# Performance work log

Hardware: AMD Instinct MI355X
Metric: run time of the kernel (lower is better)

The kernel has to match this reference:

```python
import jax, jax.numpy as jnp
import numpy as np

B, S, D = 4, 1024, 2048
NH, HD = 16, 128  # nhead, head_dim
SCALE = HD ** -0.5


def setup_inputs() -> dict:
    key = jax.random.key(0)
    ks = jax.random.split(key, 7)
    query = jax.random.normal(ks[0], (B, S, D), dtype=jnp.float32)
    key_t = jax.random.normal(ks[1], (B, S, D), dtype=jnp.float32)
    value = jax.random.normal(ks[2], (B, S, D), dtype=jnp.float32)
    # qkv_proj: Linear(D, 3D) with bias; out_proj: Linear(D, D) with bias
    Wqkv = jax.random.normal(ks[3], (3 * D, D), dtype=jnp.float32) * (D ** -0.5)
    bqkv = jnp.zeros((3 * D,), dtype=jnp.float32)
    Wout = jax.random.normal(ks[4], (D, D), dtype=jnp.float32) * (D ** -0.5)
    bout = jnp.zeros((D,), dtype=jnp.float32)
    return {"query": query, "key": key_t, "value": value,
            "Wqkv": Wqkv, "bqkv": bqkv, "Wout": Wout, "bout": bout}


def reference(query, key, value, Wqkv, bqkv, Wout, bout):
    # NOTE: module ignores `key`/`value` args; qkv comes from query alone.
    b, s, d = query.shape
    qkv = query @ Wqkv.T + bqkv                       # (B,S,3D)
    q, k, v = jnp.split(qkv, 3, axis=-1)
    q = q.reshape(b, s, NH, HD).transpose(0, 2, 1, 3) * SCALE  # (B,H,S,hd)
    k = k.reshape(b, s, NH, HD).transpose(0, 2, 1, 3)          # (B,H,S,hd)
    # faithful replication of the module's odd v permutation:
    v = v.reshape(b, s, HD, NH).transpose(0, 2, 1, 3)          # (B,hd,S,H)
    v = v.reshape(b, s, NH * HD).reshape(b, s, NH, HD).transpose(0, 2, 1, 3)  # (B,H,S,hd)
    scores = jnp.einsum('bhqd,bhkd->bhqk', q, k)               # (B,H,S,S)
    causal = jnp.triu(jnp.ones((s, s), dtype=bool), k=1)
    scores = jnp.where(causal, -jnp.inf, scores)
    attn = jax.nn.softmax(scores.astype(jnp.float32), axis=-1).astype(query.dtype)
    out = jnp.einsum('bhqk,bhkd->bhqd', attn, v)               # (B,H,S,hd)
    out = out.transpose(0, 2, 1, 3).reshape(b, s, d)
    return out @ Wout.T + bout
```

## Files before the change

### kernel.cpp

```cpp
#include <hip/hip_runtime.h>
#include <hip/hip_bf16.h>
#include <stdint.h>

typedef __bf16 bf16x8 __attribute__((ext_vector_type(8)));
typedef float  floatx4 __attribute__((ext_vector_type(4)));

#define NEG_BIG (-1e30f)

#define GLD16(g, l) __builtin_amdgcn_global_load_lds(                         \
    (__attribute__((address_space(1))) void*)(g),                             \
    (__attribute__((address_space(3))) void*)(l), 16, 0, 0)

__device__ __forceinline__ void cvt16(const float* __restrict__ s,
                                      __hip_bfloat16* __restrict__ d) {
    float4 f[4];
#pragma unroll
    for (int i = 0; i < 4; i++) f[i] = ((const float4*)s)[i];
    union { __hip_bfloat16 h[16]; uint4 u[2]; } o;
#pragma unroll
    for (int i = 0; i < 4; i++) {
        o.h[4 * i + 0] = __float2bfloat16(f[i].x);
        o.h[4 * i + 1] = __float2bfloat16(f[i].y);
        o.h[4 * i + 2] = __float2bfloat16(f[i].z);
        o.h[4 * i + 3] = __float2bfloat16(f[i].w);
    }
    ((uint4*)d)[0] = o.u[0];
    ((uint4*)d)[1] = o.u[1];
}

__global__ __launch_bounds__(256)
void cvt3_f32_bf16(const float* __restrict__ a, size_t na8,
                   const float* __restrict__ b, size_t nb8,
                   const float* __restrict__ c, size_t nc8,
                   __hip_bfloat16* __restrict__ da,
                   __hip_bfloat16* __restrict__ db,
                   __hip_bfloat16* __restrict__ dc)
{
    const size_t total  = na8 + nb8 + nc8;
    const size_t stride = (size_t)gridDim.x * blockDim.x;
    for (size_t idx = (size_t)blockIdx.x * blockDim.x + threadIdx.x;
         idx < total; idx += stride) {
        const float* s; __hip_bfloat16* d; size_t o;
        if (idx < na8)            { s = a; d = da; o = idx; }
        else if (idx < na8 + nb8) { s = b; d = db; o = idx - na8; }
        else                      { s = c; d = dc; o = idx - na8 - nb8; }
        const float4 f0 = ((const float4*)s)[o * 2 + 0];
        const float4 f1 = ((const float4*)s)[o * 2 + 1];
        union { __hip_bfloat16 h[8]; uint4 u; } z;
        z.h[0] = __float2bfloat16(f0.x); z.h[1] = __float2bfloat16(f0.y);
        z.h[2] = __float2bfloat16(f0.z); z.h[3] = __float2bfloat16(f0.w);
        z.h[4] = __float2bfloat16(f1.x); z.h[5] = __float2bfloat16(f1.y);
        z.h[6] = __float2bfloat16(f1.z); z.h[7] = __float2bfloat16(f1.w);
        ((uint4*)d)[o] = z.u;
    }
}

__global__ __launch_bounds__(256, 2)
void gemm2b_nt_bias(const __hip_bfloat16* __restrict__ A,
                    const __hip_bfloat16* __restrict__ B,
                    const float* __restrict__ bias,
                    __hip_bfloat16* __restrict__ C,
                    int M, int N, int K, int lda, int ldb)
{
    __shared__ __align__(16) __hip_bfloat16 Asm[2][128 * 64];
    __shared__ __align__(16) __hip_bfloat16 Bsm[2][192 * 64];

    const int flat = blockIdx.x;
    const int c    = flat & 7;
    const int i_   = flat >> 3;
    const int by = (c & 1) * 16 + (i_ & 15);
    const int bx = (c >> 1) * 8 + (i_ >> 4);
    const int m0 = by * 128, n0 = bx * 192;

    const int t    = threadIdx.x;
    const int wave = t >> 6, lane = t & 63;
    const int quad = lane >> 4, l16 = lane & 15;
    const int wr   = wave >> 1, wc = wave & 1;
    const int NT   = K >> 6;

    const int l8 = lane >> 3;
    const int g_ = (lane & 7) ^ l8;
    auto stageA = [&](int tk, int j, int buf) {
        GLD16(A + (size_t)(m0 + j * 32 + wave * 8 + l8) * lda + tk * 64 + g_ * 8,
              &Asm[buf][0] + (j * 32 + wave * 8) * 64);
    };
    auto stageB = [&](int tk, int j, int buf) {
        GLD16(B + (size_t)(n0 + j * 32 + wave * 8 + l8) * ldb + tk * 64 + g_ * 8,
              &Bsm[buf][0] + (j * 32 + wave * 8) * 64);
    };

    const int g0 = (quad ^ (l16 & 7)) << 3;

    floatx4 acc[4][6];
    const floatx4 zero = {0.f, 0.f, 0.f, 0.f};
#pragma unroll
    for (int mi = 0; mi < 4; mi++)
#pragma unroll
        for (int ni = 0; ni < 6; ni++) acc[mi][ni] = zero;

#pragma unroll
    for (int j = 0; j < 4; j++) stageA(0, j, 0);
#pragma unroll
    for (int j = 0; j < 6; j++) stageB(0, j, 0);
    if (NT > 1) {
        stageA(1, 0, 1); stageA(1, 2, 1);
        stageB(1, 0, 1); stageB(1, 1, 1); stageB(1, 2, 1);
        asm volatile("s_waitcnt vmcnt(5)" ::: "memory");
    } else {
        asm volatile("s_waitcnt vmcnt(0)" ::: "memory");
    }
    __syncthreads();

    int cb = 0;
    for (int tk = 0; tk < NT; ++tk, cb ^= 1) {
        const __hip_bfloat16* Ab = &Asm[cb][0];
        const __hip_bfloat16* Bb = &Bsm[cb][0];
        const int nb = cb ^ 1;

        bf16x8 af[2][2], bfr[6][2];
#pragma unroll
        for (int i = 0; i < 2; i++)
#pragma unroll
            for (int ks = 0; ks < 2; ks++)
                af[i][ks] = *(const bf16x8*)(
                    Ab + (wr * 64 + i * 16 + l16) * 64 + (g0 ^ (ks ? 32 : 0)));
#pragma unroll
        for (int ni = 0; ni < 6; ni++)
#pragma unroll
            for (int ks = 0; ks < 2; ks++)
                bfr[ni][ks] = *(const bf16x8*)(
                    Bb + (wc * 96 + ni * 16 + l16) * 64 + (g0 ^ (ks ? 32 : 0)));
        if (tk + 1 < NT) {
            stageA(tk + 1, 1, nb); stageA(tk + 1, 3, nb);
            stageB(tk + 1, 3, nb); stageB(tk + 1, 4, nb); stageB(tk + 1, 5, nb);
        }
        __builtin_amdgcn_s_barrier();
        asm volatile("s_waitcnt lgkmcnt(0)" ::: "memory");
        __builtin_amdgcn_s_setprio(1);
#pragma unroll
        for (int ks = 0; ks < 2; ks++)
#pragma unroll
            for (int i = 0; i < 2; i++)
#pragma unroll
                for (int ni = 0; ni < 6; ni++)
                    acc[i][ni] = __builtin_amdgcn_mfma_f32_16x16x32_bf16(
                        af[i][ks], bfr[ni][ks], acc[i][ni], 0, 0, 0);
        __builtin_amdgcn_s_setprio(0);
        __builtin_amdgcn_s_barrier();

#pragma unroll
        for (int i = 0; i < 2; i++)
#pragma unroll
            for (int ks = 0; ks < 2; ks++)
                af[i][ks] = *(const bf16x8*)(
                    Ab + (wr * 64 + (2 + i) * 16 + l16) * 64 + (g0 ^ (ks ? 32 : 0)));
        if (tk + 2 < NT) {
            stageA(tk + 2, 0, cb); stageA(tk + 2, 2, cb);
            stageB(tk + 2, 0, cb); stageB(tk + 2, 1, cb); stageB(tk + 2, 2, cb);
        }
        __builtin_amdgcn_s_barrier();
        asm volatile("s_waitcnt lgkmcnt(0)" ::: "memory");
        __builtin_amdgcn_s_setprio(1);
#pragma unroll
        for (int ks = 0; ks < 2; ks++)
#pragma unroll
            for (int i = 0; i < 2; i++)
#pragma unroll
                for (int ni = 0; ni < 6; ni++)
                    acc[2 + i][ni] = __builtin_amdgcn_mfma_f32_16x16x32_bf16(
                        af[i][ks], bfr[ni][ks], acc[2 + i][ni], 0, 0, 0);
        __builtin_amdgcn_s_setprio(0);
        if (tk + 2 < NT)
            asm volatile("s_waitcnt vmcnt(5)" ::: "memory");
        else if (tk + 1 < NT)
            asm volatile("s_waitcnt vmcnt(0)" ::: "memory");
        __builtin_amdgcn_s_barrier();
    }

#pragma unroll
    for (int mi = 0; mi < 4; mi++) {
        const int row = m0 + wr * 64 + mi * 16 + quad * 4;
#pragma unroll
        for (int ni = 0; ni < 6; ni++) {
            const int col = n0 + wc * 96 + ni * 16 + l16;
            const float bv = bias[col];
#pragma unroll
            for (int r = 0; r < 4; r++)
                C[(size_t)(row + r) * N + col] =
                    __float2bfloat16(acc[mi][ni][r] + bv);
        }
    }
}

__global__ __launch_bounds__(256, 2)
void gemm2b128_nt_bias(const __hip_bfloat16* __restrict__ A,
                       const __hip_bfloat16* __restrict__ B,
                       const float* __restrict__ bias,
                       float* __restrict__ C,
                       int M, int N, int K, int lda, int ldb)
{
    __shared__ __align__(16) __hip_bfloat16 Asm[2][128 * 64];
    __shared__ __align__(16) __hip_bfloat16 Bsm[2][128 * 64];

    const int flat = blockIdx.x;
    const int c    = flat & 7;
    const int i_   = flat >> 3;
    const int by = (c & 3) * 8 + (i_ & 7);
    const int bx = (c >> 2) * 8 + (i_ >> 3);
    const int m0 = by * 128, n0 = bx * 128;

    const int t    = threadIdx.x;
    const int wave = t >> 6, lane = t & 63;
    const int quad = lane >> 4, l16 = lane & 15;
    const int wr   = wave >> 1, wc = wave & 1;
    const int NT   = K >> 6;

    const int l8 = lane >> 3;
    const int g_ = (lane & 7) ^ l8;
    auto stageA = [&](int tk, int j, int buf) {
        GLD16(A + (size_t)(m0 + j * 32 + wave * 8 + l8) * lda + tk * 64 + g_ * 8,
              &Asm[buf][0] + (j * 32 + wave * 8) * 64);
    };
    auto stageB = [&](int tk, int j, int buf) {
        GLD16(B + (size_t)(n0 + j * 32 + wave * 8 + l8) * ldb + tk * 64 + g_ * 8,
              &Bsm[buf][0] + (j * 32 + wave * 8) * 64);
    };

    const int g0 = (quad ^ (l16 & 7)) << 3;

    floatx4 acc[4][4];
    const floatx4 zero = {0.f, 0.f, 0.f, 0.f};
#pragma unroll
    for (int mi = 0; mi < 4; mi++)
#pragma unroll
        for (int ni = 0; ni < 4; ni++) acc[mi][ni] = zero;

#pragma unroll
    for (int j = 0; j < 4; j++) stageA(0, j, 0);
#pragma unroll
    for (int j = 0; j < 4; j++) stageB(0, j, 0);
    if (NT > 1) {
        stageA(1, 0, 1); stageA(1, 2, 1); stageB(1, 0, 1); stageB(1, 1, 1);
        asm volatile("s_waitcnt vmcnt(4)" ::: "memory");
    } else {
        asm volatile("s_waitcnt vmcnt(0)" ::: "memory");
    }
    __syncthreads();

    int cb = 0;
    for (int tk = 0; tk < NT; ++tk, cb ^= 1) {
        const __hip_bfloat16* Ab = &Asm[cb][0];
        const __hip_bfloat16* Bb = &Bsm[cb][0];
        const int nb = cb ^ 1;

        bf16x8 af[2][2], bfr[4][2];
#pragma unroll
        for (int i = 0; i < 2; i++)
#pragma unroll
            for (int ks = 0; ks < 2; ks++)
                af[i][ks] = *(const bf16x8*)(
                    Ab + (wr * 64 + i * 16 + l16) * 64 + (g0 ^ (ks ? 32 : 0)));
#pragma unroll
        for (int ni = 0; ni < 4; ni++)
#pragma unroll
            for (int ks = 0; ks < 2; ks++)
                bfr[ni][ks] = *(const bf16x8*)(
                    Bb + (wc * 64 + ni * 16 + l16) * 64 + (g0 ^ (ks ? 32 : 0)));
        if (tk + 1 < NT) {
            stageA(tk + 1, 1, nb); stageA(tk + 1, 3, nb);
            stageB(tk + 1, 2, nb); stageB(tk + 1, 3, nb);
        }
        __builtin_amdgcn_s_barrier();
        asm volatile("s_waitcnt lgkmcnt(0)" ::: "memory");
        __builtin_amdgcn_s_setprio(1);
#pragma unroll
        for (int ks = 0; ks < 2; ks++)
#pragma unroll
            for (int i = 0; i < 2; i++)
#pragma unroll
                for (int ni = 0; ni < 4; ni++)
                    acc[i][ni] = __builtin_amdgcn_mfma_f32_16x16x32_bf16(
                        af[i][ks], bfr[ni][ks], acc[i][ni], 0, 0, 0);
        __builtin_amdgcn_s_setprio(0);
        __builtin_amdgcn_s_barrier();

#pragma unroll
        for (int i = 0; i < 2; i++)
#pragma unroll
            for (int ks = 0; ks < 2; ks++)
                af[i][ks] = *(const bf16x8*)(
                    Ab + (wr * 64 + (2 + i) * 16 + l16) * 64 + (g0 ^ (ks ? 32 : 0)));
        if (tk + 2 < NT) {
            stageA(tk + 2, 0, cb); stageA(tk + 2, 2, cb);
            stageB(tk + 2, 0, cb); stageB(tk + 2, 1, cb);
        }
        __builtin_amdgcn_s_barrier();
        asm volatile("s_waitcnt lgkmcnt(0)" ::: "memory");
        __builtin_amdgcn_s_setprio(1);
#pragma unroll
        for (int ks = 0; ks < 2; ks++)
#pragma unroll
            for (int i = 0; i < 2; i++)
#pragma unroll
                for (int ni = 0; ni < 4; ni++)
                    acc[2 + i][ni] = __builtin_amdgcn_mfma_f32_16x16x32_bf16(
                        af[i][ks], bfr[ni][ks], acc[2 + i][ni], 0, 0, 0);
        __builtin_amdgcn_s_setprio(0);
        if (tk + 2 < NT)
            asm volatile("s_waitcnt vmcnt(4)" ::: "memory");
        else if (tk + 1 < NT)
            asm volatile("s_waitcnt vmcnt(0)" ::: "memory");
        __builtin_amdgcn_s_barrier();
    }

#pragma unroll
    for (int mi = 0; mi < 4; mi++) {
        const int row = m0 + wr * 64 + mi * 16 + quad * 4;
#pragma unroll
        for (int ni = 0; ni < 4; ni++) {
            const int col = n0 + wc * 64 + ni * 16 + l16;
            const float bv = bias[col];
#pragma unroll
            for (int r = 0; r < 4; r++)
                C[(size_t)(row + r) * N + col] = acc[mi][ni][r] + bv;
        }
    }
}

template <bool A_F32, bool B_F32, bool OUT_F32>
__global__ __launch_bounds__(256, 2)
void gemm_nt_bias(const void* __restrict__ Av, const void* __restrict__ Bv,
                  const float* __restrict__ bias, void* __restrict__ Cv,
                  int M, int N, int K, int lda, int ldb)
{
    __shared__ __align__(16) __hip_bfloat16 Asm[128 * 32];
    __shared__ __align__(16) __hip_bfloat16 Bsm[128 * 32];
    const int m0   = blockIdx.y * 128;
    const int n0   = blockIdx.x * 128;
    const int t    = threadIdx.x;
    const int wave = t >> 6, lane = t & 63;
    const int quad = lane >> 4, l16 = lane & 15;
    const int wr   = wave >> 1, wc = wave & 1;

    floatx4 zero = {0.f, 0.f, 0.f, 0.f};
    floatx4 acc[4][4];
    for (int i = 0; i < 4; i++)
        for (int j = 0; j < 4; j++) acc[i][j] = zero;

    for (int k0 = 0; k0 < K; k0 += 32) {
        if (A_F32) {
            const float* A = (const float*)Av;
            const int row = t >> 1, half = t & 1;
            cvt16(A + (size_t)(m0 + row) * lda + k0 + half * 16,
                  Asm + row * 32 + half * 16);
        } else {
            const __hip_bfloat16* A = (const __hip_bfloat16*)Av;
            for (int j = 0; j < 2; ++j) {
                const int chunk = (wave * 2 + j) * 64 + lane;
                const int row   = chunk >> 2;
                const int kc    = chunk & 3;
                GLD16(A + (size_t)(m0 + row) * lda + k0 + kc * 8,
                      Asm + (wave * 2 + j) * 512);
            }
        }
        if (B_F32) {
            const float* B = (const float*)Bv;
            const int row = t >> 1, half = t & 1;
            cvt16(B + (size_t)(n0 + row) * ldb + k0 + half * 16,
                  Bsm + row * 32 + half * 16);
        } else {
            const __hip_bfloat16* B = (const __hip_bfloat16*)Bv;
            for (int j = 0; j < 2; ++j) {
                const int chunk = (wave * 2 + j) * 64 + lane;
                const int row   = chunk >> 2;
                const int kc    = chunk & 3;
                GLD16(B + (size_t)(n0 + row) * ldb + k0 + kc * 8,
                      Bsm + (wave * 2 + j) * 512);
            }
        }
        __syncthreads();

        bf16x8 af[4], bf[4];
        for (int i = 0; i < 4; i++) {
            af[i] = *(const bf16x8*)(Asm + (wr * 64 + i * 16 + l16) * 32 + quad * 8);
            bf[i] = *(const bf16x8*)(Bsm + (wc * 64 + i * 16 + l16) * 32 + quad * 8);
        }
        for (int mi = 0; mi < 4; mi++)
            for (int ni = 0; ni < 4; ni++)
                acc[mi][ni] = __builtin_amdgcn_mfma_f32_16x16x32_bf16(
                    af[mi], bf[ni], acc[mi][ni], 0, 0, 0);
        __syncthreads();
    }

    for (int mi = 0; mi < 4; mi++) {
        const int row = m0 + wr * 64 + mi * 16 + quad * 4;
        for (int ni = 0; ni < 4; ni++) {
            const int col = n0 + wc * 64 + ni * 16 + l16;
            const float bv = bias[col];
            for (int r = 0; r < 4; r++) {
                const float v = acc[mi][ni][r] + bv;
                if (OUT_F32)
                    ((float*)Cv)[(size_t)(row + r) * N + col] = v;
                else
                    ((__hip_bfloat16*)Cv)[(size_t)(row + r) * N + col] =
                        __float2bfloat16(v);
            }
        }
    }
}

__global__ __launch_bounds__(256)
void permute_v(const __hip_bfloat16* __restrict__ QKV,
               __hip_bfloat16* __restrict__ Vpt)
{
    __shared__ __align__(16) __hip_bfloat16 S[64 * 64];
    const int blk = blockIdx.x;
    const int sb = blk & 31, h = (blk >> 5) & 15, b = blk >> 9;
    const int t = threadIdx.x;

    for (int j = 0; j < 2; j++) {
        const int chunk = j * 256 + t;
        const int lrow  = chunk >> 3;
        const int lcol  = (chunk & 7) * 8;
        const int r8 = lrow >> 3, jj = lrow & 7;
        const int srow = r8 * 128 + h * 8 + jj;
        const int scol = sb * 64 + lcol;
        *(uint4*)(S + chunk * 8) =
            *(const uint4*)(QKV + ((size_t)(b * 1024) + srow) * 6144 + 4096 + scol);
    }
    __syncthreads();

    const size_t obase = (((size_t)(b * 16 + h)) * 32 + sb) * 4096;
    for (int i = 0; i < 16; i++) {
        const int lin = t + 256 * i;
        const int hd = lin >> 5, ss = lin & 31;
        Vpt[obase + lin] =
            S[((ss & 7) * 8 + (hd >> 4)) * 64 + (ss >> 3) * 16 + (hd & 15)];
    }
}

__global__ __launch_bounds__(256, 2)
void flash_attn(const __hip_bfloat16* __restrict__ QKV,
                const __hip_bfloat16* __restrict__ Vpt,
                __hip_bfloat16* __restrict__ O)
{
    __shared__ __align__(16) __hip_bfloat16 Kt[2][64 * 128];
    __shared__ __align__(16) __hip_bfloat16 Vt[2][2 * 128 * 32];
    __shared__ __align__(16) __hip_bfloat16 Pl[64 * 64];

    const int bid  = blockIdx.x;
    const int pair = bid >> 6;
    const int g    = bid & 63;
    const int b    = g >> 4, h = g & 15;
    const int t    = threadIdx.x;
    const int wave = t >> 6, lane = t & 63;
    const int quad = lane >> 4, l16 = lane & 15;
    const float scale = 0.08838834764831845f;

    const int    rowb  = b * 1024;
    const size_t vbase = (((size_t)(b * 16 + h)) * 32) * 4096;
    const floatx4 zero = {0.f, 0.f, 0.f, 0.f};

    auto stageK = [&](int tk, int bufi) {
        const int kv0 = tk * 64;
        __hip_bfloat16* dst = &Kt[bufi][0];
#pragma unroll
        for (int j = 0; j < 4; j++) {
            const int c0 = (wave * 4 + j) * 64 + lane;
            const int r  = c0 >> 4;
            const int gg = (c0 & 15) ^ (r & 7);
            GLD16(QKV + ((size_t)(rowb + kv0 + r)) * 6144 + 2048 + h * 128 + gg * 8,
                  dst + (wave * 4 + j) * 512);
        }
    };
    auto stageV = [&](int tk, int bufi) {
        const __hip_bfloat16* src = Vpt + vbase + (size_t)(tk * 2) * 4096;
        __hip_bfloat16* dst = &Vt[bufi][0];
#pragma unroll
        for (int j = 0; j < 4; j++) {
            const int c0   = (wave * 4 + j) * 64 + lane;
            const int half = c0 >> 9, w = c0 & 511;
            const int r    = w >> 2;
            const int gg   = (w & 3) ^ (r & 3);
            GLD16(src + half * 4096 + r * 32 + gg * 8,
                  dst + (wave * 4 + j) * 512);
        }
    };

    for (int ph = 0; ph < 2; ++ph) {
        const int qb = ph ? (15 - pair) * 64 : pair * 64;
        const int nt = ph ? 16 - pair       : pair + 1;

        bf16x8 qf[4];
        {
            const size_t rb = ((size_t)(rowb + qb + wave * 16 + l16)) * 6144 + h * 128;
#pragma unroll
            for (int kc = 0; kc < 4; kc++)
                qf[kc] = *(const bf16x8*)(QKV + rb + kc * 32 + quad * 8);
        }

        float m_i[4], l_i[4];
        floatx4 oacc[8];
#pragma unroll
        for (int r = 0; r < 4; r++) { m_i[r] = NEG_BIG; l_i[r] = 0.f; }
#pragma unroll
        for (int ni = 0; ni < 8; ni++) oacc[ni] = zero;

        stageK(0, 0); stageV(0, 0);

        for (int tk = 0; tk < nt; ++tk) {
            const int cur = tk & 1;
            if (tk + 1 < nt) {
                stageK(tk + 1, cur ^ 1); stageV(tk + 1, cur ^ 1);
                asm volatile("s_waitcnt vmcnt(8)" ::: "memory");
            } else {
                asm volatile("s_waitcnt vmcnt(0)" ::: "memory");
            }
            __builtin_amdgcn_s_barrier();
            asm volatile("" ::: "memory");

            const __hip_bfloat16* Kb = &Kt[cur][0];
            const __hip_bfloat16* Vb = &Vt[cur][0];
            const int kv0 = tk * 64;

            floatx4 sc[4];
#pragma unroll
            for (int cbk = 0; cbk < 4; cbk++) {
                floatx4 s = zero;
                const int r  = cbk * 16 + l16;
                const int sw = r & 7;
#pragma unroll
                for (int kc = 0; kc < 4; kc++) {
                    bf16x8 kf = *(const bf16x8*)(
                        Kb + r * 128 + (((kc * 4 + quad) ^ sw) << 3));
                    s = __builtin_amdgcn_mfma_f32_16x16x32_bf16(qf[kc], kf, s, 0, 0, 0);
                }
                sc[cbk] = s;
            }

            const int qrow = qb + wave * 16 + quad * 4;
            if (tk == nt - 1) {
#pragma unroll
                for (int rr = 0; rr < 4; rr++)
#pragma unroll
                    for (int cbk = 0; cbk < 4; cbk++) {
                        const int col = kv0 + cbk * 16 + l16;
                        const float v = sc[cbk][rr] * scale;
                        sc[cbk][rr] = (col > qrow + rr) ? NEG_BIG : v;
                    }
            } else {
#pragma unroll
                for (int rr = 0; rr < 4; rr++)
#pragma unroll
                    for (int cbk = 0; cbk < 4; cbk++) sc[cbk][rr] *= scale;
            }
            float mx[4];
#pragma unroll
            for (int rr = 0; rr < 4; rr++)
                mx[rr] = fmaxf(fmaxf(sc[0][rr], sc[1][rr]),
                               fmaxf(sc[2][rr], sc[3][rr]));
#pragma unroll
            for (int off = 1; off < 16; off <<= 1)
#pragma unroll
                for (int rr = 0; rr < 4; rr++)
                    mx[rr] = fmaxf(mx[rr], __shfl_xor(mx[rr], off));

            bool grow = false;
#pragma unroll
            for (int rr = 0; rr < 4; rr++)
                grow = grow || (mx[rr] > m_i[rr] + 8.0f);
            if (__any((int)grow)) {
#pragma unroll
                for (int rr = 0; rr < 4; rr++) {
                    const float mnew  = fmaxf(m_i[rr], mx[rr]);
                    const float alpha = __expf(m_i[rr] - mnew);
                    m_i[rr] = mnew;
                    float lsum = 0.f;
#pragma unroll
                    for (int cbk = 0; cbk < 4; cbk++) {
                        const float pv = __expf(sc[cbk][rr] - mnew);
                        sc[cbk][rr] = pv;
                        lsum += pv;
                    }
                    l_i[rr] = l_i[rr] * alpha + lsum;
#pragma unroll
                    for (int ni = 0; ni < 8; ni++) oacc[ni][rr] *= alpha;
                }
            } else {
#pragma unroll
                for (int rr = 0; rr < 4; rr++) {
                    float lsum = 0.f;
#pragma unroll
                    for (int cbk = 0; cbk < 4; cbk++) {
                        const float pv = __expf(sc[cbk][rr] - m_i[rr]);
                        sc[cbk][rr] = pv;
                        lsum += pv;
                    }
                    l_i[rr] += lsum;
                }
            }

#pragma unroll
            for (int cbk = 0; cbk < 4; cbk++)
#pragma unroll
                for (int rr = 0; rr < 4; rr++) {
                    const int row = wave * 16 + quad * 4 + rr;
                    const int col = cbk * 16 + l16;
                    Pl[row * 64 + ((((col >> 3) ^ (row & 7)) << 3) | (col & 7))] =
                        __float2bfloat16(sc[cbk][rr]);
                }
            asm volatile("s_waitcnt lgkmcnt(0)" ::: "memory");

            const int prow = wave * 16 + l16;
            bf16x8 pf[2];
#pragma unroll
            for (int kc = 0; kc < 2; kc++)
                pf[kc] = *(const bf16x8*)(
                    Pl + prow * 64 + (((kc * 4 + quad) ^ (prow & 7)) << 3));
#pragma unroll
            for (int ni = 0; ni < 8; ni++) {
                const int vr = ni * 16 + l16;
#pragma unroll
                for (int kc = 0; kc < 2; kc++) {
                    bf16x8 vf = *(const bf16x8*)(
                        Vb + kc * 4096 + vr * 32 + (((quad ^ (vr & 3))) << 3));
                    oacc[ni] = __builtin_amdgcn_mfma_f32_16x16x32_bf16(
                        pf[kc], vf, oacc[ni], 0, 0, 0);
                }
            }

            asm volatile("" ::: "memory");
            __builtin_amdgcn_s_barrier();
            asm volatile("" ::: "memory");
        }

#pragma unroll
        for (int off = 1; off < 16; off <<= 1)
#pragma unroll
            for (int rr = 0; rr < 4; rr++)
                l_i[rr] += __shfl_xor(l_i[rr], off);
        float inv[4];
#pragma unroll
        for (int rr = 0; rr < 4; rr++) inv[rr] = 1.0f / l_i[rr];
#pragma unroll
        for (int ni = 0; ni < 8; ni++)
#pragma unroll
            for (int rr = 0; rr < 4; rr++) {
                const int row = qb + wave * 16 + quad * 4 + rr;
                O[((size_t)rowb + row) * 6144 + 4096 + h * 128 + ni * 16 + l16] =
                    __float2bfloat16(oacc[ni][rr] * inv[rr]);
            }
    }
}

extern "C" void kernel_launch(void* const* d_in, const int* in_sizes, int n_in,
                              void* d_out, int out_size, void* d_ws, size_t ws_size,
                              hipStream_t stream) {
    const float* query = (const float*)d_in[0];
    const float* Wqkv = (const float*)d_in[3];
    const float* bqkv = (const float*)d_in[4];
    const float* Wout = (const float*)d_in[5];
    const float* bout = (const float*)d_in[6];
    float* out = (float*)d_out;

    const size_t MB = 1048576;
    char* ws = (char*)d_ws;
    __hip_bfloat16* QKV = (__hip_bfloat16*)ws;
    __hip_bfloat16* Vpt = (__hip_bfloat16*)(ws + 48 * MB);
    __hip_bfloat16* Att = QKV + 4096;

    dim3 blk(256);

    if (ws_size >= 113 * MB) {
        __hip_bfloat16* Qbf     = (__hip_bfloat16*)(ws + 64 * MB);
        __hip_bfloat16* Wqkv_bf = (__hip_bfloat16*)(ws + 80 * MB);
        __hip_bfloat16* Wout_bf = (__hip_bfloat16*)(ws + 104 * MB);

        cvt3_f32_bf16<<<dim3(2048), blk, 0, stream>>>(
            query, (size_t)4096 * 2048 / 8,
            Wqkv,  (size_t)6144 * 2048 / 8,
            Wout,  (size_t)2048 * 2048 / 8,
            Qbf, Wqkv_bf, Wout_bf);
        gemm2b_nt_bias<<<dim3(1024), dim3(256), 0, stream>>>(
            Qbf, Wqkv_bf, bqkv, QKV, 4096, 6144, 2048, 2048, 2048);
        permute_v<<<dim3(2048), blk, 0, stream>>>(QKV, Vpt);
        flash_attn<<<dim3(512), blk, 0, stream>>>(QKV, Vpt, QKV);
        gemm2b128_nt_bias<<<dim3(512), dim3(256), 0, stream>>>(
            Att, Wout_bf, bout, out, 4096, 2048, 2048, 6144, 2048);
    } else {
        gemm_nt_bias<true, true, false><<<dim3(48, 32), blk, 0, stream>>>(
            query, Wqkv, bqkv, QKV, 4096, 6144, 2048, 2048, 2048);
        permute_v<<<dim3(2048), blk, 0, stream>>>(QKV, Vpt);
        flash_attn<<<dim3(512), blk, 0, stream>>>(QKV, Vpt, QKV);
        gemm_nt_bias<false, true, true><<<dim3(16, 32), blk, 0, stream>>>(
            Att, Wout, bout, out, 4096, 2048, 2048, 6144, 2048);
    }
}
```

Measured before the change: 354.9 us.

## Halve GEMM K-tile to 32 to fit four blocks per CU

Both bf16 GEMMs (QKV projection and output projection) now stage K-tiles of 32 instead of 64, which halves shared memory per block. Launch bounds are raised to allow four resident blocks per CU. The pipeline is simplified to one compute phase per tile, with a two-tiles-ahead prefetch issued right after the fragment reads, and the LDS swizzle is adjusted to the narrower rows. This aims to hide latency through higher occupancy, at the cost of twice as many barriers and loop iterations and tighter register budgets that could cause spills.

```diff
diff --git a/kernel.cpp b/kernel.cpp
--- a/kernel.cpp
+++ b/kernel.cpp
@@ -55,15 +55,15 @@
     }
 }
 
-__global__ __launch_bounds__(256, 2)
-void gemm2b_nt_bias(const __hip_bfloat16* __restrict__ A,
+__global__ __launch_bounds__(256, 4)
+void gemm4b_nt_bias(const __hip_bfloat16* __restrict__ A,
                     const __hip_bfloat16* __restrict__ B,
                     const float* __restrict__ bias,
                     __hip_bfloat16* __restrict__ C,
                     int M, int N, int K, int lda, int ldb)
 {
-    __shared__ __align__(16) __hip_bfloat16 Asm[2][128 * 64];
-    __shared__ __align__(16) __hip_bfloat16 Bsm[2][192 * 64];
+    __shared__ __align__(16) __hip_bfloat16 Asm[2][128 * 32];
+    __shared__ __align__(16) __hip_bfloat16 Bsm[2][192 * 32];
 
     const int flat = blockIdx.x;
     const int c    = flat & 7;
@@ -76,20 +76,22 @@
     const int wave = t >> 6, lane = t & 63;
     const int quad = lane >> 4, l16 = lane & 15;
     const int wr   = wave >> 1, wc = wave & 1;
-    const int NT   = K >> 6;
-
-    const int l8 = lane >> 3;
-    const int g_ = (lane & 7) ^ l8;
+    const int NT   = K >> 5;
+
+    const int rloc = lane >> 2;
+    const int g_   = (lane & 3) ^ (rloc & 3);
     auto stageA = [&](int tk, int j, int buf) {
-        GLD16(A + (size_t)(m0 + j * 32 + wave * 8 + l8) * lda + tk * 64 + g_ * 8,
-              &Asm[buf][0] + (j * 32 + wave * 8) * 64);
+        const int row = j * 64 + wave * 16 + rloc;
+        GLD16(A + (size_t)(m0 + row) * lda + tk * 32 + g_ * 8,
+              &Asm[buf][0] + (j * 64 + wave * 16) * 32);
     };
     auto stageB = [&](int tk, int j, int buf) {
-        GLD16(B + (size_t)(n0 + j * 32 + wave * 8 + l8) * ldb + tk * 64 + g_ * 8,
-              &Bsm[buf][0] + (j * 32 + wave * 8) * 64);
+        const int row = j * 64 + wave * 16 + rloc;
+        GLD16(B + (size_t)(n0 + row) * ldb + tk * 32 + g_ * 8,
+              &Bsm[buf][0] + (j * 64 + wave * 16) * 32);
     };
 
-    const int g0 = (quad ^ (l16 & 7)) << 3;
+    const int g0 = (quad ^ (l16 & 3)) << 3;
 
     floatx4 acc[4][6];
     const floatx4 zero = {0.f, 0.f, 0.f, 0.f};
@@ -99,12 +101,14 @@
         for (int ni = 0; ni < 6; ni++) acc[mi][ni] = zero;
 
 #pragma unroll
-    for (int j = 0; j < 4; j++) stageA(0, j, 0);
-#pragma unroll
-    for (int j = 0; j < 6; j++) stageB(0, j, 0);
+    for (int j = 0; j < 2; j++) stageA(0, j, 0);
+#pragma unroll
+    for (int j = 0; j < 3; j++) stageB(0, j, 0);
     if (NT > 1) {
-        stageA(1, 0, 1); stageA(1, 2, 1);
-        stageB(1, 0, 1); stageB(1, 1, 1); stageB(1, 2, 1);
+#pragma unroll
+        for (int j = 0; j < 2; j++) stageA(1, j, 1);
+#pragma unroll
+        for (int j = 0; j < 3; j++) stageB(1, j, 1);
         asm volatile("s_waitcnt vmcnt(5)" ::: "memory");
     } else {
         asm volatile("s_waitcnt vmcnt(0)" ::: "memory");
@@ -115,60 +119,30 @@
     for (int tk = 0; tk < NT; ++tk, cb ^= 1) {
         const __hip_bfloat16* Ab = &Asm[cb][0];
         const __hip_bfloat16* Bb = &Bsm[cb][0];
-        const int nb = cb ^ 1;
-
-        bf16x8 af[2][2], bfr[6][2];
-#pragma unroll
-        for (int i = 0; i < 2; i++)
-#pragma unroll
-            for (int ks = 0; ks < 2; ks++)
-                af[i][ks] = *(const bf16x8*)(
-                    Ab + (wr * 64 + i * 16 + l16) * 64 + (g0 ^ (ks ? 32 : 0)));
+
+        bf16x8 af[4], bfr[6];
+#pragma unroll
+        for (int i = 0; i < 4; i++)
+            af[i] = *(const bf16x8*)(Ab + (wr * 64 + i * 16 + l16) * 32 + g0);
 #pragma unroll
         for (int ni = 0; ni < 6; ni++)
-#pragma unroll
-            for (int ks = 0; ks < 2; ks++)
-                bfr[ni][ks] = *(const bf16x8*)(
-                    Bb + (wc * 96 + ni * 16 + l16) * 64 + (g0 ^ (ks ? 32 : 0)));
-        if (tk + 1 < NT) {
-            stageA(tk + 1, 1, nb); stageA(tk + 1, 3, nb);
-            stageB(tk + 1, 3, nb); stageB(tk + 1, 4, nb); stageB(tk + 1, 5, nb);
-        }
+            bfr[ni] = *(const bf16x8*)(Bb + (wc * 96 + ni * 16 + l16) * 32 + g0);
+
         __builtin_amdgcn_s_barrier();
         asm volatile("s_waitcnt lgkmcnt(0)" ::: "memory");
+        if (tk + 2 < NT) {
+#pragma unroll
+            for (int j = 0; j < 2; j++) stageA(tk + 2, j, cb);
+#pragma unroll
+            for (int j = 0; j < 3; j++) stageB(tk + 2, j, cb);
+        }
         __builtin_amdgcn_s_setprio(1);
 #pragma unroll
-        for (int ks = 0; ks < 2; ks++)
-#pragma unroll
-            for (int i = 0; i < 2; i++)
-#pragma unroll
-                for (int ni = 0; ni < 6; ni++)
-                    acc[i][ni] = __builtin_amdgcn_mfma_f32_16x16x32_bf16(
-                        af[i][ks], bfr[ni][ks], acc[i][ni], 0, 0, 0);
-        __builtin_amdgcn_s_setprio(0);
-        __builtin_amdgcn_s_barrier();
-
-#pragma unroll
-        for (int i = 0; i < 2; i++)
-#pragma unroll
-            for (int ks = 0; ks < 2; ks++)
-                af[i][ks] = *(const bf16x8*)(
-                    Ab + (wr * 64 + (2 + i) * 16 + l16) * 64 + (g0 ^ (ks ? 32 : 0)));
-        if (tk + 2 < NT) {
-            stageA(tk + 2, 0, cb); stageA(tk + 2, 2, cb);
-            stageB(tk + 2, 0, cb); stageB(tk + 2, 1, cb); stageB(tk + 2, 2, cb);
-        }
-        __builtin_amdgcn_s_barrier();
-        asm volatile("s_waitcnt lgkmcnt(0)" ::: "memory");
-        __builtin_amdgcn_s_setprio(1);
-#pragma unroll
-        for (int ks = 0; ks < 2; ks++)
-#pragma unroll
-            for (int i = 0; i < 2; i++)
-#pragma unroll
-                for (int ni = 0; ni < 6; ni++)
-                    acc[2 + i][ni] = __builtin_amdgcn_mfma_f32_16x16x32_bf16(
-                        af[i][ks], bfr[ni][ks], acc[2 + i][ni], 0, 0, 0);
+        for (int i = 0; i < 4; i++)
+#pragma unroll
+            for (int ni = 0; ni < 6; ni++)
+                acc[i][ni] = __builtin_amdgcn_mfma_f32_16x16x32_bf16(
+                    af[i], bfr[ni], acc[i][ni], 0, 0, 0);
         __builtin_amdgcn_s_setprio(0);
         if (tk + 2 < NT)
             asm volatile("s_waitcnt vmcnt(5)" ::: "memory");
@@ -192,15 +166,15 @@
     }
 }
 
-__global__ __launch_bounds__(256, 2)
-void gemm2b128_nt_bias(const __hip_bfloat16* __restrict__ A,
+__global__ __launch_bounds__(256, 4)
+void gemm4b128_nt_bias(const __hip_bfloat16* __restrict__ A,
                        const __hip_bfloat16* __restrict__ B,
                        const float* __restrict__ bias,
                        float* __restrict__ C,
                        int M, int N, int K, int lda, int ldb)
 {
-    __shared__ __align__(16) __hip_bfloat16 Asm[2][128 * 64];
-    __shared__ __align__(16) __hip_bfloat16 Bsm[2][128 * 64];
+    __shared__ __align__(16) __hip_bfloat16 Asm[2][128 * 32];
+    __shared__ __align__(16) __hip_bfloat16 Bsm[2][128 * 32];
 
     const int flat = blockIdx.x;
     const int c    = flat & 7;
@@ -213,20 +187,22 @@
     const int wave = t >> 6, lane = t & 63;
     const int quad = lane >> 4, l16 = lane & 15;
     const int wr   = wave >> 1, wc = wave & 1;
-    const int NT   = K >> 6;
-
-    const int l8 = lane >> 3;
-    const int g_ = (lane & 7) ^ l8;
+    const int NT   = K >> 5;
+
+    const int rloc = lane >> 2;
+    const int g_   = (lane & 3) ^ (rloc & 3);
     auto stageA = [&](int tk, int j, int buf) {
-        GLD16(A + (size_t)(m0 + j * 32 + wave * 8 + l8) * lda + tk * 64 + g_ * 8,
-              &Asm[buf][0] + (j * 32 + wave * 8) * 64);
+        const int row = j * 64 + wave * 16 + rloc;
+        GLD16(A + (size_t)(m0 + row) * lda + tk * 32 + g_ * 8,
+              &Asm[buf][0] + (j * 64 + wave * 16) * 32);
     };
     auto stageB = [&](int tk, int j, int buf) {
-        GLD16(B + (size_t)(n0 + j * 32 + wave * 8 + l8) * ldb + tk * 64 + g_ * 8,
-              &Bsm[buf][0] + (j * 32 + wave * 8) * 64);
+        const int row = j * 64 + wave * 16 + rloc;
+        GLD16(B + (size_t)(n0 + row) * ldb + tk * 32 + g_ * 8,
+              &Bsm[buf][0] + (j * 64 + wave * 16) * 32);
     };
 
-    const int g0 = (quad ^ (l16 & 7)) << 3;
+    const int g0 = (quad ^ (l16 & 3)) << 3;
 
     floatx4 acc[4][4];
     const floatx4 zero = {0.f, 0.f, 0.f, 0.f};
@@ -236,11 +212,10 @@
         for (int ni = 0; ni < 4; ni++) acc[mi][ni] = zero;
 
 #pragma unroll
-    for (int j = 0; j < 4; j++) stageA(0, j, 0);
-#pragma unroll
-    for (int j = 0; j < 4; j++) stageB(0, j, 0);
+    for (int j = 0; j < 2; j++) { stageA(0, j, 0); stageB(0, j, 0); }
     if (NT > 1) {
-        stageA(1, 0, 1); stageA(1, 2, 1); stageB(1, 0, 1); stageB(1, 1, 1);
+#pragma unroll
+        for (int j = 0; j < 2; j++) { stageA(1, j, 1); stageB(1, j, 1); }
         asm volatile("s_waitcnt vmcnt(4)" ::: "memory");
     } else {
         asm volatile("s_waitcnt vmcnt(0)" ::: "memory");
@@ -251,60 +226,28 @@
     for (int tk = 0; tk < NT; ++tk, cb ^= 1) {
         const __hip_bfloat16* Ab = &Asm[cb][0];
         const __hip_bfloat16* Bb = &Bsm[cb][0];
-        const int nb = cb ^ 1;
-
-        bf16x8 af[2][2], bfr[4][2];
-#pragma unroll
-        for (int i = 0; i < 2; i++)
-#pragma unroll
-            for (int ks = 0; ks < 2; ks++)
-                af[i][ks] = *(const bf16x8*)(
-                    Ab + (wr * 64 + i * 16 + l16) * 64 + (g0 ^ (ks ? 32 : 0)));
+
+        bf16x8 af[4], bfr[4];
+#pragma unroll
+        for (int i = 0; i < 4; i++)
+            af[i] = *(const bf16x8*)(Ab + (wr * 64 + i * 16 + l16) * 32 + g0);
 #pragma unroll
         for (int ni = 0; ni < 4; ni++)
-#pragma unroll
-            for (int ks = 0; ks < 2; ks++)
-                bfr[ni][ks] = *(const bf16x8*)(
-                    Bb + (wc * 64 + ni * 16 + l16) * 64 + (g0 ^ (ks ? 32 : 0)));
-        if (tk + 1 < NT) {
-            stageA(tk + 1, 1, nb); stageA(tk + 1, 3, nb);
-            stageB(tk + 1, 2, nb); stageB(tk + 1, 3, nb);
-        }
+            bfr[ni] = *(const bf16x8*)(Bb + (wc * 64 + ni * 16 + l16) * 32 + g0);
+
         __builtin_amdgcn_s_barrier();
         asm volatile("s_waitcnt lgkmcnt(0)" ::: "memory");
+        if (tk + 2 < NT) {
+#pragma unroll
+            for (int j = 0; j < 2; j++) { stageA(tk + 2, j, cb); stageB(tk + 2, j, cb); }
+        }
         __builtin_amdgcn_s_setprio(1);
 #pragma unroll
-        for (int ks = 0; ks < 2; ks++)
-#pragma unroll
-            for (int i = 0; i < 2; i++)
-#pragma unroll
-                for (int ni = 0; ni < 4; ni++)
-                    acc[i][ni] = __builtin_amdgcn_mfma_f32_16x16x32_bf16(
-                        af[i][ks], bfr[ni][ks], acc[i][ni], 0, 0, 0);
-        __builtin_amdgcn_s_setprio(0);
-        __builtin_amdgcn_s_barrier();
-
-#pragma unroll
-        for (int i = 0; i < 2; i++)
-#pragma unroll
-            for (int ks = 0; ks < 2; ks++)
-                af[i][ks] = *(const bf16x8*)(
-                    Ab + (wr * 64 + (2 + i) * 16 + l16) * 64 + (g0 ^ (ks ? 32 : 0)));
-        if (tk + 2 < NT) {
-            stageA(tk + 2, 0, cb); stageA(tk + 2, 2, cb);
-            stageB(tk + 2, 0, cb); stageB(tk + 2, 1, cb);
-        }
-        __builtin_amdgcn_s_barrier();
-        asm volatile("s_waitcnt lgkmcnt(0)" ::: "memory");
-        __builtin_amdgcn_s_setprio(1);
-#pragma unroll
-        for (int ks = 0; ks < 2; ks++)
-#pragma unroll
-            for (int i = 0; i < 2; i++)
-#pragma unroll
-                for (int ni = 0; ni < 4; ni++)
-                    acc[2 + i][ni] = __builtin_amdgcn_mfma_f32_16x16x32_bf16(
-                        af[i][ks], bfr[ni][ks], acc[2 + i][ni], 0, 0, 0);
+        for (int i = 0; i < 4; i++)
+#pragma unroll
+            for (int ni = 0; ni < 4; ni++)
+                acc[i][ni] = __builtin_amdgcn_mfma_f32_16x16x32_bf16(
+                    af[i], bfr[ni], acc[i][ni], 0, 0, 0);
         __builtin_amdgcn_s_setprio(0);
         if (tk + 2 < NT)
             asm volatile("s_waitcnt vmcnt(4)" ::: "memory");
@@ -681,11 +624,11 @@
             Wqkv,  (size_t)6144 * 2048 / 8,
             Wout,  (size_t)2048 * 2048 / 8,
             Qbf, Wqkv_bf, Wout_bf);
-        gemm2b_nt_bias<<<dim3(1024), dim3(256), 0, stream>>>(
+        gemm4b_nt_bias<<<dim3(1024), dim3(256), 0, stream>>>(
             Qbf, Wqkv_bf, bqkv, QKV, 4096, 6144, 2048, 2048, 2048);
         permute_v<<<dim3(2048), blk, 0, stream>>>(QKV, Vpt);
         flash_attn<<<dim3(512), blk, 0, stream>>>(QKV, Vpt, QKV);
-        gemm2b128_nt_bias<<<dim3(512), dim3(256), 0, stream>>>(
+        gemm4b128_nt_bias<<<dim3(512), dim3(256), 0, stream>>>(
             Att, Wout_bf, bout, out, 4096, 2048, 2048, 6144, 2048);
     } else {
         gemm_nt_bias<true, true, false><<<dim3(48, 32), blk, 0, stream>>>(
```

Measured after the change: 763.3 us. 2.15x slower.
